# Kernel tuning notes

Hardware: AMD Instinct MI355X
Metric: run time of the kernel (lower is better)

Reference implementation:

```python
import jax, jax.numpy as jnp
import numpy as np
import math

B, D_MODEL, H, D_K, L = 24, 128, 8, 16, 512


def setup_inputs() -> dict:
    key = jax.random.key(0)
    ks = jax.random.split(key, 5)
    x = jax.random.normal(ks[0], (B, D_MODEL, L), dtype=jnp.float32)
    Wq = jax.random.normal(ks[1], (H, B, D_K, D_MODEL), dtype=jnp.float32)
    Wk = jax.random.normal(ks[2], (H, B, D_K, D_MODEL), dtype=jnp.float32)
    Wv = jax.random.normal(ks[3], (H, B, D_K, D_MODEL), dtype=jnp.float32)
    Wo = jax.random.normal(ks[4], (B, H * D_K, D_MODEL), dtype=jnp.float32)
    return {"x": x, "Wq": Wq, "Wk": Wk, "Wv": Wv, "Wo": Wo}


def reference(x, Wq, Wk, Wv, Wo):
    # Per-head, per-batch projections: [h,b,k,d] @ [b,d,l] -> [h,b,k,l]
    Q = jnp.einsum('hbkd,bdl->hbkl', Wq, x)
    K = jnp.einsum('hbkd,bdl->hbkl', Wk, x)
    V = jnp.einsum('hbkd,bdl->hbkl', Wv, x)
    # scores[h,b,l,m] = Q[:, :, :, l] . K[:, :, :, m]; torch softmax dim=1 of
    # the [B, L, L] score -> softmax over the QUERY axis l (axis=2 here).
    scores = jnp.einsum('hbkl,hbkm->hblm', Q, K) / math.sqrt(D_K)
    attn = jax.nn.softmax(scores, axis=2)
    # head_i = V @ attn : [h,b,v,l] @ [h,b,l,m] -> [h,b,v,m]
    heads = jnp.einsum('hbvl,hblm->hbvm', V, attn)
    # concat heads along channel dim: [b, h*v, L]
    head = heads.transpose(1, 0, 2, 3).reshape(B, H * D_K, L)
    # out = Wo @ head : [b, h*v, d_model] treated as [b,128,128] @ [b,128,L]
    out = jnp.einsum('bod,bdl->bol', Wo, head)
    return out
```

## Files before the change

kernel.cpp:

```cpp
#include <hip/hip_runtime.h>
#include <math.h>

#define NB 24
#define DM 128
#define NH 8
#define DK 16
#define LL 512
#define HB (NH * NB)

#define XTH_OFF 0
#define XTL_OFF 3145728
#define HT_OFF  6291456

typedef __attribute__((ext_vector_type(8))) short bf16x8;
typedef __attribute__((ext_vector_type(4))) float f32x4;
typedef __attribute__((ext_vector_type(4))) int   i32x4;

#define MFMA  __builtin_amdgcn_mfma_f32_16x16x32_bf16
#define EXP2  __builtin_amdgcn_exp2f

static __device__ __forceinline__ unsigned bfr(float x) {
    return (__float_as_uint(x) + 0x8000u) & 0xffff0000u;
}

static __device__ __forceinline__ unsigned cvtpk(float a, float b) {
    unsigned r;
    asm("v_cvt_pk_bf16_f32 %0, %1, %2" : "=v"(r) : "v"(a), "v"(b));
    return r;
}

static __device__ __forceinline__ void wsplit(const float* __restrict__ p,
                                              bf16x8& aH, bf16x8& aL) {
    const float4 f0 = *(const float4*)p;
    const float4 f1 = *(const float4*)(p + 4);
    const float f[8] = {f0.x, f0.y, f0.z, f0.w, f1.x, f1.y, f1.z, f1.w};
    i32x4 h, l;
    #pragma unroll
    for (int q = 0; q < 4; ++q) {
        const unsigned h0 = bfr(f[2 * q]), h1 = bfr(f[2 * q + 1]);
        const unsigned e0 = bfr(f[2 * q]     - __uint_as_float(h0));
        const unsigned e1 = bfr(f[2 * q + 1] - __uint_as_float(h1));
        h[q] = (int)((h0 >> 16) | (h1 & 0xffff0000u));
        l[q] = (int)((e0 >> 16) | (e1 & 0xffff0000u));
    }
    aH = __builtin_bit_cast(bf16x8, h);
    aL = __builtin_bit_cast(bf16x8, l);
}

__global__ __launch_bounds__(256)
void prep(const float* __restrict__ x,
          unsigned short* __restrict__ xthi,
          unsigned short* __restrict__ xtlo)
{
    __shared__ float T[64][65];
    const int bid = blockIdx.x, tid = threadIdx.x;
    const int b = bid >> 3, lc = bid & 7;

    #pragma unroll
    for (int half = 0; half < 2; ++half) {
        const int d0 = half << 6;
        const float* __restrict__ xb =
            x + (size_t)b * 65536 + (size_t)d0 * LL + lc * 64;
        if (half) __syncthreads();
        #pragma unroll
        for (int i = 0; i < 16; ++i) {
            const int idx = i * 256 + tid;
            T[idx >> 6][idx & 63] = xb[(size_t)(idx >> 6) * LL + (idx & 63)];
        }
        __syncthreads();
        #pragma unroll
        for (int i = 0; i < 8; ++i) {
            const int idx = (i * 256 + tid) * 2;
            const int l = idx >> 6, dd = idx & 63;
            const float v0 = T[dd][l], v1 = T[dd + 1][l];
            const unsigned h0 = bfr(v0), h1 = bfr(v1);
            const unsigned e0 = bfr(v0 - __uint_as_float(h0));
            const unsigned e1 = bfr(v1 - __uint_as_float(h1));
            const size_t o = (size_t)b * 65536 +
                             (size_t)(lc * 64 + l) * DM + d0 + dd;
            *(unsigned*)(xthi + o) = (h0 >> 16) | (h1 & 0xffff0000u);
            *(unsigned*)(xtlo + o) = (e0 >> 16) | (e1 & 0xffff0000u);
        }
    }
}

static __device__ __forceinline__ void pv_acc(
    const f32x4& s0, const f32x4& s1, float M, float& sm,
    f32x4& O, const bf16x8& aV)
{
    const float e0 = EXP2(s0[0] - M), e1 = EXP2(s0[1] - M);
    const float e2 = EXP2(s0[2] - M), e3 = EXP2(s0[3] - M);
    const float e4 = EXP2(s1[0] - M), e5 = EXP2(s1[1] - M);
    const float e6 = EXP2(s1[2] - M), e7 = EXP2(s1[3] - M);
    sm += ((e0 + e1) + (e2 + e3)) + ((e4 + e5) + (e6 + e7));
    i32x4 bi = { (int)cvtpk(e0, e1), (int)cvtpk(e2, e3),
                 (int)cvtpk(e4, e5), (int)cvtpk(e6, e7) };
    O = MFMA(aV, __builtin_bit_cast(bf16x8, bi), O, 0, 0, 0);
}

#define QK_STRIDE 42
#define V_STRIDE  520

__global__ __launch_bounds__(512)
void qkv_attn(const unsigned short* __restrict__ xthi,
              const unsigned short* __restrict__ xtlo,
              const float* __restrict__ Wq,
              const float* __restrict__ Wk,
              const float* __restrict__ Wv,
              unsigned short* __restrict__ ht)
{
    __shared__ unsigned short qs[LL * QK_STRIDE];
    __shared__ unsigned short ks[LL * QK_STRIDE];
    __shared__ unsigned short vs[DK * V_STRIDE];

    const int hb    = blockIdx.x;
    const int b     = hb % NB;
    const int wv    = threadIdx.x >> 6;
    const int lane  = threadIdx.x & 63;
    const int g     = lane >> 4;
    const int mR    = lane & 15;
    const int lQ    = wv * 64;

    {
        const float* __restrict__ wqp = Wq + (size_t)hb * 2048 + mR * 128 + g * 8;
        const float* __restrict__ wkp = Wk + (size_t)hb * 2048 + mR * 128 + g * 8;
        const float* __restrict__ wvp = Wv + (size_t)hb * 2048 + mR * 128 + g * 8;
        const unsigned short* __restrict__ xh = xthi + (size_t)b * 65536 + g * 8;
        const unsigned short* __restrict__ xl = xtlo + (size_t)b * 65536 + g * 8;

        f32x4 CQ[4], CK[4], CV[4];
        #pragma unroll
        for (int t = 0; t < 4; ++t) {
            CQ[t] = (f32x4){0.f, 0.f, 0.f, 0.f};
            CK[t] = (f32x4){0.f, 0.f, 0.f, 0.f};
            CV[t] = (f32x4){0.f, 0.f, 0.f, 0.f};
        }

        #pragma unroll
        for (int kk = 0; kk < 4; ++kk) {
            bf16x8 bH[4], bL[4];
            #pragma unroll
            for (int t = 0; t < 4; ++t) {
                const size_t ro = (size_t)(lQ + t * 16 + mR) * DM + kk * 32;
                bH[t] = *(const bf16x8*)(xh + ro);
                bL[t] = *(const bf16x8*)(xl + ro);
            }
            bf16x8 aH, aL;
            wsplit(wqp + kk * 32, aH, aL);
            #pragma unroll
            for (int t = 0; t < 4; ++t) {
                CQ[t] = MFMA(aH, bH[t], CQ[t], 0, 0, 0);
                CQ[t] = MFMA(aH, bL[t], CQ[t], 0, 0, 0);
                CQ[t] = MFMA(aL, bH[t], CQ[t], 0, 0, 0);
            }
            wsplit(wkp + kk * 32, aH, aL);
            #pragma unroll
            for (int t = 0; t < 4; ++t) {
                CK[t] = MFMA(aH, bH[t], CK[t], 0, 0, 0);
                CK[t] = MFMA(aH, bL[t], CK[t], 0, 0, 0);
                CK[t] = MFMA(aL, bH[t], CK[t], 0, 0, 0);
            }
            wsplit(wvp + kk * 32, aH, aL);
            #pragma unroll
            for (int t = 0; t < 4; ++t) {
                CV[t] = MFMA(aH, bH[t], CV[t], 0, 0, 0);
                CV[t] = MFMA(aH, bL[t], CV[t], 0, 0, 0);
                CV[t] = MFMA(aL, bH[t], CV[t], 0, 0, 0);
            }
        }

        #pragma unroll
        for (int t = 0; t < 4; ++t) {
            const int l = lQ + t * 16 + mR;
            #pragma unroll
            for (int i = 0; i < 4; ++i)
                vs[(4 * g + i) * V_STRIDE + l] =
                    (unsigned short)(bfr(CV[t][i]) >> 16);
        }
        #pragma unroll
        for (int t = 0; t < 4; ++t) {
            const int l = lQ + t * 16 + mR;
            ushort4 hi4, lo4;
            #pragma unroll
            for (int i = 0; i < 4; ++i) {
                const float v = CQ[t][i];
                const unsigned h = bfr(v);
                const unsigned lw = bfr(v - __uint_as_float(h));
                ((unsigned short*)&hi4)[i] = (unsigned short)(h >> 16);
                ((unsigned short*)&lo4)[i] = (unsigned short)(lw >> 16);
            }
            *(ushort4*)(qs + l * QK_STRIDE + 4 * g)      = hi4;
            *(ushort4*)(qs + l * QK_STRIDE + 16 + 4 * g) = lo4;
        }
        #pragma unroll
        for (int t = 0; t < 4; ++t) {
            const int r = lQ + t * 16 + mR;
            ushort4 hi4, lo4;
            #pragma unroll
            for (int i = 0; i < 4; ++i) {
                const float v = CK[t][i] * (0.25f * 1.44269504f);
                const unsigned h = bfr(v);
                const unsigned lw = bfr(v - __uint_as_float(h));
                ((unsigned short*)&hi4)[i] = (unsigned short)(h >> 16);
                ((unsigned short*)&lo4)[i] = (unsigned short)(lw >> 16);
            }
            *(ushort4*)(ks + r * QK_STRIDE + 4 * g)      = hi4;
            *(ushort4*)(ks + r * QK_STRIDE + 16 + 4 * g) = lo4;
        }
    }

    __syncthreads();

    bf16x8 K0[2], K0s[2], K1[2], K1s[2];
    #pragma unroll
    for (int sub = 0; sub < 2; ++sub) {
        const unsigned short* Kr0 = ks + (lQ + sub * 32 + mR) * QK_STRIDE;
        const unsigned short* Kr1 = Kr0 + 16 * QK_STRIDE;
        K0[sub]  = *(const bf16x8*)(Kr0 + g * 8);
        K0s[sub] = *(const bf16x8*)(Kr0 + (g ^ 2) * 8);
        K1[sub]  = *(const bf16x8*)(Kr1 + g * 8);
        K1s[sub] = *(const bf16x8*)(Kr1 + (g ^ 2) * 8);
    }

    const int rA = 8 * (mR >> 2) + (mR & 3);
    const unsigned short* qrowA = qs + rA * QK_STRIDE + g * 8;
    const unsigned short* qrowB = qrowA + 4 * QK_STRIDE;
    const unsigned short* vrow  = vs + mR * V_STRIDE + g * 8;

    float MA[2] = {-1e30f, -1e30f}, MB[2] = {-1e30f, -1e30f};
    for (int l = 0; l < LL; l += 32) {
        const bf16x8 aQ0 = *(const bf16x8*)(qrowA + l * QK_STRIDE);
        const bf16x8 aQ1 = *(const bf16x8*)(qrowB + l * QK_STRIDE);
        #pragma unroll
        for (int sub = 0; sub < 2; ++sub) {
            const f32x4 z = {0.f,0.f,0.f,0.f};
            const f32x4 sA0 = MFMA(aQ0, K0[sub], z, 0,0,0);
            const f32x4 sB0 = MFMA(aQ0, K1[sub], z, 0,0,0);
            const f32x4 sA1 = MFMA(aQ1, K0[sub], z, 0,0,0);
            const f32x4 sB1 = MFMA(aQ1, K1[sub], z, 0,0,0);
            float tmA = fmaxf(fmaxf(fmaxf(sA0[0],sA0[1]), fmaxf(sA0[2],sA0[3])),
                              fmaxf(fmaxf(sA1[0],sA1[1]), fmaxf(sA1[2],sA1[3])));
            float tmB = fmaxf(fmaxf(fmaxf(sB0[0],sB0[1]), fmaxf(sB0[2],sB0[3])),
                              fmaxf(fmaxf(sB1[0],sB1[1]), fmaxf(sB1[2],sB1[3])));
            MA[sub] = fmaxf(MA[sub], tmA);
            MB[sub] = fmaxf(MB[sub], tmB);
        }
    }
    #pragma unroll
    for (int sub = 0; sub < 2; ++sub) {
        MA[sub] = fmaxf(MA[sub], __shfl_xor(MA[sub], 16, 64));
        MA[sub] = fmaxf(MA[sub], __shfl_xor(MA[sub], 32, 64));
        MB[sub] = fmaxf(MB[sub], __shfl_xor(MB[sub], 16, 64));
        MB[sub] = fmaxf(MB[sub], __shfl_xor(MB[sub], 32, 64));
    }

    f32x4 O[2][2];
    float smA[2] = {0.f, 0.f}, smB[2] = {0.f, 0.f};
    #pragma unroll
    for (int sub = 0; sub < 2; ++sub)
        #pragma unroll
        for (int gr = 0; gr < 2; ++gr)
            O[sub][gr] = (f32x4){0.f, 0.f, 0.f, 0.f};

    for (int l = 0; l < LL; l += 32) {
        const bf16x8 aQ0 = *(const bf16x8*)(qrowA + l * QK_STRIDE);
        const bf16x8 aQ1 = *(const bf16x8*)(qrowB + l * QK_STRIDE);
        const bf16x8 aV  = *(const bf16x8*)(vrow + l);

        #pragma unroll
        for (int sub = 0; sub < 2; ++sub) {
            const f32x4 z = {0.f,0.f,0.f,0.f};
            f32x4 sA0 = MFMA(aQ0, K0[sub], z, 0,0,0);
            sA0 = MFMA(aQ0, K0s[sub], sA0, 0,0,0);
            f32x4 sB0 = MFMA(aQ0, K1[sub], z, 0,0,0);
            sB0 = MFMA(aQ0, K1s[sub], sB0, 0,0,0);
            f32x4 sA1 = MFMA(aQ1, K0[sub], z, 0,0,0);
            sA1 = MFMA(aQ1, K0s[sub], sA1, 0,0,0);
            f32x4 sB1 = MFMA(aQ1, K1[sub], z, 0,0,0);
            sB1 = MFMA(aQ1, K1s[sub], sB1, 0,0,0);

            pv_acc(sA0, sA1, MA[sub], smA[sub], O[sub][0], aV);
            pv_acc(sB0, sB1, MB[sub], smB[sub], O[sub][1], aV);
        }
    }

    const int h = hb / NB, bb = hb % NB;
    #pragma unroll
    for (int sub = 0; sub < 2; ++sub) {
        float s0 = smA[sub], s1 = smB[sub];
        s0 += __shfl_xor(s0, 16, 64);  s0 += __shfl_xor(s0, 32, 64);
        s1 += __shfl_xor(s1, 16, 64);  s1 += __shfl_xor(s1, 32, 64);
        const float i0 = 1.f / s0, i1 = 1.f / s1;

        unsigned short* __restrict__ ho =
            ht + (size_t)bb * 65536 +
            (size_t)(lQ + sub * 32 + mR) * DM + h * 16 + 4 * g;
        ushort4 p0, p1;
        #pragma unroll
        for (int i = 0; i < 4; ++i) {
            ((unsigned short*)&p0)[i] =
                (unsigned short)(bfr(O[sub][0][i] * i0) >> 16);
            ((unsigned short*)&p1)[i] =
                (unsigned short)(bfr(O[sub][1][i] * i1) >> 16);
        }
        *(ushort4*)ho             = p0;
        *(ushort4*)(ho + 16 * DM) = p1;
    }
}

__global__ __launch_bounds__(256)
void out_mfma(const float* __restrict__ Wo,
              const unsigned short* __restrict__ ht,
              float* __restrict__ out)
{
    const int blk  = blockIdx.x;
    const int b    = blk >> 5;
    const int mq   = (blk >> 4) & 1;
    const int nq   = blk & 15;
    const int wv   = threadIdx.x >> 6;
    const int lane = threadIdx.x & 63;
    const int g = lane >> 4, mR = lane & 15;
    const int m0 = (mq * 4 + wv) * 16;
    const int n0 = nq * 32;

    const float* __restrict__ A =
        Wo + (size_t)b * 16384 + (size_t)(m0 + mR) * DM + g * 8;
    const unsigned short* __restrict__ B = ht + (size_t)b * 65536 + g * 8;

    f32x4 C0 = {0.f,0.f,0.f,0.f}, C1 = {0.f,0.f,0.f,0.f};
    #pragma unroll
    for (int kk = 0; kk < 4; ++kk) {
        const float4 f0 = *(const float4*)(A + kk * 32);
        const float4 f1 = *(const float4*)(A + kk * 32 + 4);
        i32x4 w;
        w[0] = (int)cvtpk(f0.x, f0.y);
        w[1] = (int)cvtpk(f0.z, f0.w);
        w[2] = (int)cvtpk(f1.x, f1.y);
        w[3] = (int)cvtpk(f1.z, f1.w);
        const bf16x8 aW = __builtin_bit_cast(bf16x8, w);
        const bf16x8 b0 = *(const bf16x8*)(B + (size_t)(n0 + mR) * DM + kk * 32);
        const bf16x8 b1 = *(const bf16x8*)(B + (size_t)(n0 + 16 + mR) * DM + kk * 32);
        C0 = MFMA(aW, b0, C0, 0, 0, 0);
        C1 = MFMA(aW, b1, C1, 0, 0, 0);
    }

    float* __restrict__ ob = out + (size_t)b * 65536 + (size_t)(m0 + 4 * g) * LL;
    #pragma unroll
    for (int i = 0; i < 4; ++i) {
        ob[(size_t)i * LL + n0 + mR]      = C0[i];
        ob[(size_t)i * LL + n0 + 16 + mR] = C1[i];
    }
}

extern "C" void kernel_launch(void* const* d_in, const int* in_sizes, int n_in,
                              void* d_out, int out_size, void* d_ws, size_t ws_size,
                              hipStream_t stream) {
    const float* x  = (const float*)d_in[0];
    const float* Wq = (const float*)d_in[1];
    const float* Wk = (const float*)d_in[2];
    const float* Wv = (const float*)d_in[3];
    const float* Wo = (const float*)d_in[4];
    float* out = (float*)d_out;

    char* ws = (char*)d_ws;
    unsigned short* xthi = (unsigned short*)(ws + XTH_OFF);
    unsigned short* xtlo = (unsigned short*)(ws + XTL_OFF);
    unsigned short* ht   = (unsigned short*)(ws + HT_OFF);

    prep     <<<192,     256, 0, stream>>>(x, xthi, xtlo);
    qkv_attn <<<HB,      512, 0, stream>>>(xthi, xtlo, Wq, Wk, Wv, ht);
    out_mfma <<<NB * 32, 256, 0, stream>>>(Wo, ht, out);
}
```

Before: 113.8 us.

## Move Q staging from LDS to global workspace to cut shared memory use

Q (split into bf16 hi/lo) is now written to a global workspace buffer instead of a large LDS array, so per-block shared memory drops by about 43 KB and more blocks can be resident per CU. Both attention loops then read Q fragments from global memory (mostly L2-cached) and are unrolled by 4 to hide that latency. The trade-off is extra global traffic and higher-latency Q loads in the inner loops. A block's waves read Q rows written by other waves, and correctness relies on the existing __syncthreads making those global writes visible across the block.

```diff
diff --git a/kernel.cpp b/kernel.cpp
--- a/kernel.cpp
+++ b/kernel.cpp
@@ -10,7 +10,8 @@
 
 #define XTH_OFF 0
 #define XTL_OFF 3145728
-#define HT_OFF  6291456
+#define QB_OFF  6291456
+#define HT_OFF  12582912
 
 typedef __attribute__((ext_vector_type(8))) short bf16x8;
 typedef __attribute__((ext_vector_type(4))) float f32x4;
@@ -107,9 +108,9 @@
               const float* __restrict__ Wq,
               const float* __restrict__ Wk,
               const float* __restrict__ Wv,
+              unsigned short* __restrict__ qb,
               unsigned short* __restrict__ ht)
 {
-    __shared__ unsigned short qs[LL * QK_STRIDE];
     __shared__ unsigned short ks[LL * QK_STRIDE];
     __shared__ unsigned short vs[DK * V_STRIDE];
 
@@ -121,6 +122,8 @@
     const int mR    = lane & 15;
     const int lQ    = wv * 64;
 
+    unsigned short* __restrict__ qg = qb + (size_t)hb * LL * 32;
+
     {
         const float* __restrict__ wqp = Wq + (size_t)hb * 2048 + mR * 128 + g * 8;
         const float* __restrict__ wkp = Wk + (size_t)hb * 2048 + mR * 128 + g * 8;
@@ -189,8 +192,8 @@
                 ((unsigned short*)&hi4)[i] = (unsigned short)(h >> 16);
                 ((unsigned short*)&lo4)[i] = (unsigned short)(lw >> 16);
             }
-            *(ushort4*)(qs + l * QK_STRIDE + 4 * g)      = hi4;
-            *(ushort4*)(qs + l * QK_STRIDE + 16 + 4 * g) = lo4;
+            *(ushort4*)(qg + (size_t)l * 32 + 4 * g)      = hi4;
+            *(ushort4*)(qg + (size_t)l * 32 + 16 + 4 * g) = lo4;
         }
         #pragma unroll
         for (int t = 0; t < 4; ++t) {
@@ -223,14 +226,15 @@
     }
 
     const int rA = 8 * (mR >> 2) + (mR & 3);
-    const unsigned short* qrowA = qs + rA * QK_STRIDE + g * 8;
-    const unsigned short* qrowB = qrowA + 4 * QK_STRIDE;
+    const unsigned short* qrowA = qg + (size_t)rA * 32 + g * 8;
+    const unsigned short* qrowB = qrowA + 4 * 32;
     const unsigned short* vrow  = vs + mR * V_STRIDE + g * 8;
 
     float MA[2] = {-1e30f, -1e30f}, MB[2] = {-1e30f, -1e30f};
+    #pragma unroll 4
     for (int l = 0; l < LL; l += 32) {
-        const bf16x8 aQ0 = *(const bf16x8*)(qrowA + l * QK_STRIDE);
-        const bf16x8 aQ1 = *(const bf16x8*)(qrowB + l * QK_STRIDE);
+        const bf16x8 aQ0 = *(const bf16x8*)(qrowA + (size_t)l * 32);
+        const bf16x8 aQ1 = *(const bf16x8*)(qrowB + (size_t)l * 32);
         #pragma unroll
         for (int sub = 0; sub < 2; ++sub) {
             const f32x4 z = {0.f,0.f,0.f,0.f};
@@ -238,12 +242,12 @@
             const f32x4 sB0 = MFMA(aQ0, K1[sub], z, 0,0,0);
             const f32x4 sA1 = MFMA(aQ1, K0[sub], z, 0,0,0);
             const f32x4 sB1 = MFMA(aQ1, K1[sub], z, 0,0,0);
-            float tmA = fmaxf(fmaxf(fmaxf(sA0[0],sA0[1]), fmaxf(sA0[2],sA0[3])),
-                              fmaxf(fmaxf(sA1[0],sA1[1]), fmaxf(sA1[2],sA1[3])));
-            float tmB = fmaxf(fmaxf(fmaxf(sB0[0],sB0[1]), fmaxf(sB0[2],sB0[3])),
-                              fmaxf(fmaxf(sB1[0],sB1[1]), fmaxf(sB1[2],sB1[3])));
-            MA[sub] = fmaxf(MA[sub], tmA);
-            MB[sub] = fmaxf(MB[sub], tmB);
+            const float tA = fmaxf(fmaxf(fmaxf(sA0[0],sA0[1]), fmaxf(sA0[2],sA0[3])),
+                                   fmaxf(fmaxf(sA1[0],sA1[1]), fmaxf(sA1[2],sA1[3])));
+            const float tB = fmaxf(fmaxf(fmaxf(sB0[0],sB0[1]), fmaxf(sB0[2],sB0[3])),
+                                   fmaxf(fmaxf(sB1[0],sB1[1]), fmaxf(sB1[2],sB1[3])));
+            MA[sub] = fmaxf(MA[sub], tA);
+            MB[sub] = fmaxf(MB[sub], tB);
         }
     }
     #pragma unroll
@@ -262,9 +266,10 @@
         for (int gr = 0; gr < 2; ++gr)
             O[sub][gr] = (f32x4){0.f, 0.f, 0.f, 0.f};
 
+    #pragma unroll 4
     for (int l = 0; l < LL; l += 32) {
-        const bf16x8 aQ0 = *(const bf16x8*)(qrowA + l * QK_STRIDE);
-        const bf16x8 aQ1 = *(const bf16x8*)(qrowB + l * QK_STRIDE);
+        const bf16x8 aQ0 = *(const bf16x8*)(qrowA + (size_t)l * 32);
+        const bf16x8 aQ1 = *(const bf16x8*)(qrowB + (size_t)l * 32);
         const bf16x8 aV  = *(const bf16x8*)(vrow + l);
 
         #pragma unroll
@@ -365,9 +370,10 @@
     char* ws = (char*)d_ws;
     unsigned short* xthi = (unsigned short*)(ws + XTH_OFF);
     unsigned short* xtlo = (unsigned short*)(ws + XTL_OFF);
+    unsigned short* qb   = (unsigned short*)(ws + QB_OFF);
     unsigned short* ht   = (unsigned short*)(ws + HT_OFF);
 
     prep     <<<192,     256, 0, stream>>>(x, xthi, xtlo);
-    qkv_attn <<<HB,      512, 0, stream>>>(xthi, xtlo, Wq, Wk, Wv, ht);
+    qkv_attn <<<HB,      512, 0, stream>>>(xthi, xtlo, Wq, Wk, Wv, qb, ht);
     out_mfma <<<NB * 32, 256, 0, stream>>>(Wo, ht, out);
 }
```

Result: no change. 113.4 us (-0.4%).
